# Optimization experiments

Measured on AMD Instinct MI355X. Metric: run time of the kernel, lower is better.

The kernel has to match this reference:

```python
import jax, jax.numpy as jnp
import numpy as np

DIM = 512
HEADS = 8
HEAD_DIM = DIM // HEADS
SR = 2
LN_EPS = 1e-3  # keras LayerNormalization default epsilon


def setup_inputs() -> dict:
    key = jax.random.key(0)
    ks = jax.random.split(key, 12)
    B, N = 4, 64 * 64
    s = lambda fan_in: 1.0 / np.sqrt(fan_in)
    return {
        "x": jax.random.normal(ks[0], (B, N, DIM), dtype=jnp.float32),
        "H": 64,
        "W": 64,
        "Wq": jax.random.normal(ks[1], (DIM, DIM), jnp.float32) * s(DIM),
        "bq": jnp.zeros((DIM,), jnp.float32),
        "Wkv": jax.random.normal(ks[2], (DIM, 2 * DIM), jnp.float32) * s(DIM),
        "bkv": jnp.zeros((2 * DIM,), jnp.float32),
        "Wp": jax.random.normal(ks[3], (DIM, DIM), jnp.float32) * s(DIM),
        "bp": jnp.zeros((DIM,), jnp.float32),
        "sr_kernel": jax.random.normal(ks[4], (SR, SR, DIM, DIM), jnp.float32) * s(SR * SR * DIM),
        "sr_bias": jnp.zeros((DIM,), jnp.float32),
        "gamma": jnp.ones((DIM,), jnp.float32),
        "beta": jnp.zeros((DIM,), jnp.float32),
    }


def _layer_norm(x, gamma, beta):
    mu = jnp.mean(x, axis=-1, keepdims=True)
    var = jnp.mean(jnp.square(x - mu), axis=-1, keepdims=True)
    return (x - mu) * jax.lax.rsqrt(var + LN_EPS) * gamma + beta


def reference(x, H, W, Wq, bq, Wkv, bkv, Wp, bp, sr_kernel, sr_bias, gamma, beta):
    B, N, C = x.shape
    scale = HEAD_DIM ** -0.5

    # q projection -> [B, heads, N, head_dim]
    q = (x @ Wq + bq).reshape(B, N, HEADS, HEAD_DIM).transpose(0, 2, 1, 3)

    # sequence reduction: strided conv (kernel=stride=SR, SAME padding) + LayerNorm
    x_ = x.reshape(B, H, W, C)
    x_ = jax.lax.conv_general_dilated(
        x_, sr_kernel, window_strides=(SR, SR), padding="SAME",
        dimension_numbers=("NHWC", "HWIO", "NHWC")) + sr_bias
    x_ = x_.reshape(B, -1, C)           # [B, N_kv, C]
    x_ = _layer_norm(x_, gamma, beta)

    # kv projection -> k, v: [B, heads, N_kv, head_dim]
    kv = (x_ @ Wkv + bkv).reshape(B, -1, 2, HEADS, HEAD_DIM).transpose(2, 0, 3, 1, 4)
    k, v = kv[0], kv[1]

    attn = jnp.einsum("bhnd,bhmd->bhnm", q, k) * scale
    attn = jax.nn.softmax(attn, axis=-1)
    out = jnp.einsum("bhnm,bhmd->bhnd", attn, v)  # [B, heads, N, head_dim]
    out = out.transpose(0, 2, 1, 3).reshape(B, N, C)
    return out @ Wp + bp
```

## Files before the change

### kernel.cpp

```cpp
#include <hip/hip_runtime.h>
#include <math.h>

#define BDIM   4
#define NTOK   4096
#define CDIM   512
#define NHEADS 8
#define HDIM   64
#define NKV    1024
#define HPIX   64
#define WPIX   64

typedef __attribute__((ext_vector_type(8)))  short    short8;
typedef __attribute__((ext_vector_type(4)))  float    floatx4;
typedef __attribute__((ext_vector_type(16))) float    floatx16;
typedef __attribute__((ext_vector_type(4)))  unsigned uintx4;
typedef unsigned short ushort_t;

static __device__ inline unsigned short f2bf(float f) {
  unsigned u = __float_as_uint(f);
  unsigned r = (u + 0x7fffu + ((u >> 16) & 1u)) >> 16;
  return (unsigned short)r;
}

static __device__ inline unsigned cvt_pk_bf16(float lo, float hi) {
  unsigned r;
  asm volatile("v_cvt_pk_bf16_f32 %0, %1, %2" : "=v"(r) : "v"(lo), "v"(hi));
  return r;
}

static __device__ inline void pl32_swap(unsigned& a, unsigned& b) {
  asm volatile("v_permlane32_swap_b32 %0, %1" : "+v"(a), "+v"(b));
}

static __device__ inline void gload16(const void* g, void* l) {
  __builtin_amdgcn_global_load_lds(
      (const __attribute__((address_space(1))) void*)g,
      (__attribute__((address_space(3))) void*)l, 16, 0, 0);
}

__global__ __launch_bounds__(256) void prep_kernel(
    const float* __restrict__ x, ushort_t* __restrict__ xb,
    const float* __restrict__ Wq, const float* __restrict__ Wkv,
    const float* __restrict__ Wp, const float* __restrict__ srk,
    ushort_t* __restrict__ Wqt, ushort_t* __restrict__ Wkvt,
    ushort_t* __restrict__ Wpt, ushort_t* __restrict__ srkt) {
  const int bid = blockIdx.x;
  if (bid < 4096) {
    const size_t i = ((size_t)bid * 256 + threadIdx.x) * 8;
    float4 f0 = *(const float4*)&x[i];
    float4 f1 = *(const float4*)&x[i + 4];
    short8 v;
    v[0] = (short)f2bf(f0.x); v[1] = (short)f2bf(f0.y);
    v[2] = (short)f2bf(f0.z); v[3] = (short)f2bf(f0.w);
    v[4] = (short)f2bf(f1.x); v[5] = (short)f2bf(f1.y);
    v[6] = (short)f2bf(f1.z); v[7] = (short)f2bf(f1.w);
    *(short8*)&xb[i] = v;
    return;
  }
  __shared__ float t[32][33];
  const int tb = bid - 4096;
  const float* in; ushort_t* outp; int C, tile;
  if (tb < 256)       { in = Wq;  outp = Wqt;  C = 512;  tile = tb; }
  else if (tb < 768)  { in = Wkv; outp = Wkvt; C = 1024; tile = tb - 256; }
  else if (tb < 1024) { in = Wp;  outp = Wpt;  C = 512;  tile = tb - 768; }
  else                { in = srk; outp = srkt; C = 512;  tile = tb - 1024; }
  const int R = (tb >= 1024) ? 2048 : 512;
  const int tcn = C >> 5;
  const int r0 = (tile / tcn) * 32, c0 = (tile % tcn) * 32;
  const int tr = threadIdx.x & 31, tc = threadIdx.x >> 5;
#pragma unroll
  for (int i = 0; i < 4; ++i)
    t[tc + 8 * i][tr] = in[(size_t)(r0 + tc + 8 * i) * C + c0 + tr];
  __syncthreads();
#pragma unroll
  for (int i = 0; i < 4; ++i)
    outp[(size_t)(c0 + tc + 8 * i) * R + r0 + tr] = f2bf(t[tr][tc + 8 * i]);
}

__global__ __launch_bounds__(256) void gemm_bf16(
    const ushort_t* __restrict__ A, const ushort_t* __restrict__ Bt,
    const float* __restrict__ bias, float* __restrict__ Cf,
    ushort_t* __restrict__ Cb, int M, int N, int K, float scale) {
  __shared__ char As[16384];
  __shared__ char Bs[16384];
  const int tid = threadIdx.x;
  const int w = tid >> 6, lane = tid & 63;
  const int g = lane >> 4, qr = lane & 15;
  const int wr = w >> 1, wc = w & 1;
  const int row0 = blockIdx.x * 128, col0 = blockIdx.y * 128;
  const int rl = w * 8 + (lane >> 3);
  const int sch = (lane & 7) ^ ((lane >> 3) & 7);

  floatx4 acc[4][4] = {};

  for (int k0 = 0; k0 < K; k0 += 64) {
    __syncthreads();
#pragma unroll
    for (int i = 0; i < 4; ++i) {
      const int r = rl + 32 * i;
      const unsigned lb = (unsigned)(w * 1024 + i * 4096);
      gload16(&A[(size_t)(row0 + r) * K + k0 + sch * 8], As + lb);
      gload16(&Bt[(size_t)(col0 + r) * K + k0 + sch * 8], Bs + lb);
    }
    __syncthreads();

#pragma unroll
    for (int kc = 0; kc < 2; ++kc) {
      short8 af[4], bfr[4];
#pragma unroll
      for (int mi = 0; mi < 4; ++mi) {
        const int r = wr * 64 + mi * 16 + qr;
        af[mi] = *(const short8*)(As +
            ((unsigned)(r * 128 + kc * 64 + g * 16) ^ (unsigned)((r & 7) << 4)));
      }
#pragma unroll
      for (int ni = 0; ni < 4; ++ni) {
        const int c = wc * 64 + ni * 16 + qr;
        bfr[ni] = *(const short8*)(Bs +
            ((unsigned)(c * 128 + kc * 64 + g * 16) ^ (unsigned)((c & 7) << 4)));
      }
#pragma unroll
      for (int mi = 0; mi < 4; ++mi)
#pragma unroll
        for (int ni = 0; ni < 4; ++ni)
          acc[mi][ni] = __builtin_amdgcn_mfma_f32_16x16x32_bf16(
              af[mi], bfr[ni], acc[mi][ni], 0, 0, 0);
    }
  }

#pragma unroll
  for (int mi = 0; mi < 4; ++mi) {
#pragma unroll
    for (int ni = 0; ni < 4; ++ni) {
      const int col = col0 + wc * 64 + ni * 16 + qr;
      const float bv = bias[col];
#pragma unroll
      for (int ri = 0; ri < 4; ++ri) {
        const int row = row0 + wr * 64 + mi * 16 + g * 4 + ri;
        const float v = (acc[mi][ni][ri] + bv) * scale;
        if (Cb) Cb[(size_t)row * N + col] = f2bf(v);
        else    Cf[(size_t)row * N + col] = v;
      }
    }
  }
}

__global__ __launch_bounds__(256) void qconv_gemm(
    const ushort_t* __restrict__ xb, const ushort_t* __restrict__ srkt,
    const float* __restrict__ srb, float* __restrict__ XR,
    const ushort_t* __restrict__ Wqt, const float* __restrict__ bq,
    ushort_t* __restrict__ Qb, float qscale) {
  __shared__ char As[16384];
  __shared__ char Bs[16384];
  const int tid = threadIdx.x;
  const int w = tid >> 6, lane = tid & 63;
  const int g = lane >> 4, qr = lane & 15;
  const int wr = w >> 1, wc = w & 1;
  const int rl = w * 8 + (lane >> 3);
  const int sch = (lane & 7) ^ ((lane >> 3) & 7);

  if (blockIdx.x < 256) {
    const int cb = blockIdx.x;
    const int row0 = (cb & 31) * 128, col0 = (cb >> 5) * 64;
    floatx4 acc[4][2] = {};

    for (int k0 = 0; k0 < 2048; k0 += 64) {
      __syncthreads();
      {
        const int di = k0 >> 10, dj = (k0 >> 9) & 1, cib = (k0 & 511) + sch * 8;
#pragma unroll
        for (int i = 0; i < 4; ++i) {
          const int r = rl + 32 * i;
          const int gr = row0 + r;
          const int bb = gr >> 10, p = gr & 1023;
          const int oi = p >> 5, oj = p & 31;
          const size_t off =
              ((size_t)((bb * HPIX + 2 * oi + di) * WPIX + 2 * oj + dj)) * CDIM + cib;
          gload16(&xb[off], As + (unsigned)(w * 1024 + i * 4096));
        }
#pragma unroll
        for (int i = 0; i < 2; ++i) {
          const int r = rl + 32 * i;
          gload16(&srkt[(size_t)(col0 + r) * 2048 + k0 + sch * 8],
                  Bs + (unsigned)(w * 1024 + i * 4096));
        }
      }
      __syncthreads();

#pragma unroll
      for (int kc = 0; kc < 2; ++kc) {
        short8 af[4], bfr[2];
#pragma unroll
        for (int mi = 0; mi < 4; ++mi) {
          const int r = wr * 64 + mi * 16 + qr;
          af[mi] = *(const short8*)(As +
              ((unsigned)(r * 128 + kc * 64 + g * 16) ^ (unsigned)((r & 7) << 4)));
        }
#pragma unroll
        for (int ni = 0; ni < 2; ++ni) {
          const int c = wc * 32 + ni * 16 + qr;
          bfr[ni] = *(const short8*)(Bs +
              ((unsigned)(c * 128 + kc * 64 + g * 16) ^ (unsigned)((c & 7) << 4)));
        }
#pragma unroll
        for (int mi = 0; mi < 4; ++mi)
#pragma unroll
          for (int ni = 0; ni < 2; ++ni)
            acc[mi][ni] = __builtin_amdgcn_mfma_f32_16x16x32_bf16(
                af[mi], bfr[ni], acc[mi][ni], 0, 0, 0);
      }
    }

#pragma unroll
    for (int mi = 0; mi < 4; ++mi) {
#pragma unroll
      for (int ni = 0; ni < 2; ++ni) {
        const int col = col0 + wc * 32 + ni * 16 + qr;
        const float bv = srb[col];
#pragma unroll
        for (int ri = 0; ri < 4; ++ri) {
          const int row = row0 + wr * 64 + mi * 16 + g * 4 + ri;
          XR[(size_t)row * 512 + col] = acc[mi][ni][ri] + bv;
        }
      }
    }
  } else {
    const int qb = blockIdx.x - 256;
    const int row0 = (qb & 127) * 128, col0 = (qb >> 7) * 128;
    floatx4 acc[4][4] = {};

    for (int k0 = 0; k0 < 512; k0 += 64) {
      __syncthreads();
#pragma unroll
      for (int i = 0; i < 4; ++i) {
        const int r = rl + 32 * i;
        const unsigned lb = (unsigned)(w * 1024 + i * 4096);
        gload16(&xb[(size_t)(row0 + r) * 512 + k0 + sch * 8], As + lb);
        gload16(&Wqt[(size_t)(col0 + r) * 512 + k0 + sch * 8], Bs + lb);
      }
      __syncthreads();

#pragma unroll
      for (int kc = 0; kc < 2; ++kc) {
        short8 af[4], bfr[4];
#pragma unroll
        for (int mi = 0; mi < 4; ++mi) {
          const int r = wr * 64 + mi * 16 + qr;
          af[mi] = *(const short8*)(As +
              ((unsigned)(r * 128 + kc * 64 + g * 16) ^ (unsigned)((r & 7) << 4)));
        }
#pragma unroll
        for (int ni = 0; ni < 4; ++ni) {
          const int c = wc * 64 + ni * 16 + qr;
          bfr[ni] = *(const short8*)(Bs +
              ((unsigned)(c * 128 + kc * 64 + g * 16) ^ (unsigned)((c & 7) << 4)));
        }
#pragma unroll
        for (int mi = 0; mi < 4; ++mi)
#pragma unroll
          for (int ni = 0; ni < 4; ++ni)
            acc[mi][ni] = __builtin_amdgcn_mfma_f32_16x16x32_bf16(
                af[mi], bfr[ni], acc[mi][ni], 0, 0, 0);
      }
    }

#pragma unroll
    for (int mi = 0; mi < 4; ++mi) {
#pragma unroll
      for (int ni = 0; ni < 4; ++ni) {
        const int col = col0 + wc * 64 + ni * 16 + qr;
        const float bv = bq[col];
#pragma unroll
        for (int ri = 0; ri < 4; ++ri) {
          const int row = row0 + wr * 64 + mi * 16 + g * 4 + ri;
          Qb[(size_t)row * 512 + col] = f2bf((acc[mi][ni][ri] + bv) * qscale);
        }
      }
    }
  }
}

__global__ __launch_bounds__(256) void gemm_kv(
    const ushort_t* __restrict__ A, const ushort_t* __restrict__ Bt,
    const float* __restrict__ bias, char* __restrict__ Kimg,
    char* __restrict__ Vimg) {
  __shared__ char As[16384];
  __shared__ char Bs[16384];
  const int tid = threadIdx.x;
  const int w = tid >> 6, lane = tid & 63;
  const int g = lane >> 4, qr = lane & 15;
  const int wr = w >> 1, wc = w & 1;
  const int row0 = blockIdx.x * 128, col0 = blockIdx.y * 128;
  const int rl = w * 8 + (lane >> 3);
  const int sch = (lane & 7) ^ ((lane >> 3) & 7);

  floatx4 acc[4][4] = {};

  for (int k0 = 0; k0 < 512; k0 += 64) {
    __syncthreads();
#pragma unroll
    for (int i = 0; i < 4; ++i) {
      const int r = rl + 32 * i;
      const unsigned lb = (unsigned)(w * 1024 + i * 4096);
      gload16(&A[(size_t)(row0 + r) * 512 + k0 + sch * 8], As + lb);
      gload16(&Bt[(size_t)(col0 + r) * 512 + k0 + sch * 8], Bs + lb);
    }
    __syncthreads();

#pragma unroll
    for (int kc = 0; kc < 2; ++kc) {
      short8 af[4], bfr[4];
#pragma unroll
      for (int mi = 0; mi < 4; ++mi) {
        const int r = wr * 64 + mi * 16 + qr;
        af[mi] = *(const short8*)(As +
            ((unsigned)(r * 128 + kc * 64 + g * 16) ^ (unsigned)((r & 7) << 4)));
      }
#pragma unroll
      for (int ni = 0; ni < 4; ++ni) {
        const int c = wc * 64 + ni * 16 + qr;
        bfr[ni] = *(const short8*)(Bs +
            ((unsigned)(c * 128 + kc * 64 + g * 16) ^ (unsigned)((c & 7) << 4)));
      }
#pragma unroll
      for (int mi = 0; mi < 4; ++mi)
#pragma unroll
        for (int ni = 0; ni < 4; ++ni)
          acc[mi][ni] = __builtin_amdgcn_mfma_f32_16x16x32_bf16(
              af[mi], bfr[ni], acc[mi][ni], 0, 0, 0);
    }
  }

#pragma unroll
  for (int mi = 0; mi < 4; ++mi) {
#pragma unroll
    for (int ni = 0; ni < 4; ++ni) {
      const int col = col0 + wc * 64 + ni * 16 + qr;
      const float bv = bias[col];
#pragma unroll
      for (int ri = 0; ri < 4; ++ri) {
        const int row = row0 + wr * 64 + mi * 16 + g * 4 + ri;
        const ushort_t v = f2bf(acc[mi][ni][ri] + bv);
        const int b = row >> 10, m = row & 1023;
        const int t = m >> 6, mr = m & 63;
        const int st = mr >> 5;
        if (col < 512) {
          const int h = col >> 6, d = col & 63;
          const int ql = mr & 31;
          const int ks = d >> 4, hi2 = (d >> 3) & 1, j = d & 7;
          char* img = Kimg + (((size_t)(b * NHEADS + h) * 16 + t) << 13);
          *(ushort_t*)(img + (unsigned)(((st * 4 + ks) << 10) +
                       ((hi2 << 5) + ql) * 16 + j * 2)) = v;
        } else {
          const int c = col - 512, h = c >> 6, d = c & 63;
          const int r5 = mr & 31;
          const int hf16 = r5 >> 4, rem = r5 & 15;
          const int hi2 = rem >> 3, cc = (rem >> 1) & 3, odd = rem & 1;
          const int db = d >> 5, ql = d & 31;
          char* img = Vimg + (((size_t)(b * NHEADS + h) * 16 + t) << 13);
          *(ushort_t*)(img + (unsigned)(((st * 4 + db * 2 + hf16) << 10) +
                       ((hi2 << 5) + ql) * 16 + cc * 4 + odd * 2)) = v;
        }
      }
    }
  }
}

__global__ __launch_bounds__(256) void ln_kernel(
    const float* __restrict__ in, ushort_t* __restrict__ out,
    const float* __restrict__ gamma, const float* __restrict__ beta) {
  const int row = blockIdx.x * 4 + (threadIdx.x >> 6);
  const int lane = threadIdx.x & 63;
  const float* p = in + (size_t)row * CDIM;
  float v[8];
  float s = 0.f;
#pragma unroll
  for (int j = 0; j < 8; ++j) { v[j] = p[lane + j * 64]; s += v[j]; }
#pragma unroll
  for (int o = 32; o > 0; o >>= 1) s += __shfl_xor(s, o);
  const float mu = s * (1.0f / 512.0f);
  float vs = 0.f;
#pragma unroll
  for (int j = 0; j < 8; ++j) { const float d = v[j] - mu; vs += d * d; }
#pragma unroll
  for (int o = 32; o > 0; o >>= 1) vs += __shfl_xor(vs, o);
  const float rstd = rsqrtf(vs * (1.0f / 512.0f) + 1e-3f);
  ushort_t* q = out + (size_t)row * CDIM;
#pragma unroll
  for (int j = 0; j < 8; ++j) {
    const int c = lane + j * 64;
    q[c] = f2bf((v[j] - mu) * rstd * gamma[c] + beta[c]);
  }
}

__global__ __launch_bounds__(256) void attn_kernel(
    const ushort_t* __restrict__ Q, const char* __restrict__ Kimg,
    const char* __restrict__ Vimg, ushort_t* __restrict__ AO) {
  __shared__ char Ks[16384];
  __shared__ char Vt[16384];

  const int b = blockIdx.z, h = blockIdx.y;
  const int q0 = blockIdx.x * 128;
  const int tid = threadIdx.x;
  const int w = tid >> 6, lane = tid & 63;
  const int ql = lane & 31;
  const int hi = lane >> 5;
  const unsigned lbyte = (unsigned)(lane * 16);

  short8 qf[4];
  {
    const ushort_t* qp = &Q[((size_t)(b * NTOK + q0 + 32 * w + ql)) * CDIM + h * HDIM];
#pragma unroll
    for (int ks = 0; ks < 4; ++ks)
      qf[ks] = *(const short8*)&qp[ks * 16 + hi * 8];
  }

  short8 ones;
#pragma unroll
  for (int i = 0; i < 8; ++i) ones[i] = (short)0x3F80;

  const char* kbase = Kimg + (((size_t)(b * NHEADS + h)) << 17);
  const char* vbase = Vimg + (((size_t)(b * NHEADS + h)) << 17);

  floatx16 Oacc[2] = {};
  floatx16 Lacc = {};

  for (int t2 = 0; t2 < NKV / 128; ++t2) {
    __syncthreads();
    {
      const char* kg = kbase + ((size_t)t2 << 14) + w * 4096 + lane * 16;
      const char* vg = vbase + ((size_t)t2 << 14) + w * 4096 + lane * 16;
      char* kd = Ks + w * 4096;
      char* vd = Vt + w * 4096;
#pragma unroll
      for (int i = 0; i < 4; ++i) {
        gload16(kg + i * 1024, kd + i * 1024);
        gload16(vg + i * 1024, vd + i * 1024);
      }
    }
    __syncthreads();

#pragma unroll
    for (int sub = 0; sub < 2; ++sub) {
      const char* ksb = Ks + sub * 8192 + lbyte;
      const char* vtb = Vt + sub * 8192 + lbyte;

      floatx16 sacc[2];
      __builtin_amdgcn_s_setprio(1);
#pragma unroll
      for (int st = 0; st < 2; ++st) {
        floatx16 s_ = {};
#pragma unroll
        for (int ks = 0; ks < 4; ++ks) {
          short8 kf = *(const short8*)(ksb + ((st * 4 + ks) << 10));
          s_ = __builtin_amdgcn_mfma_f32_32x32x16_bf16(kf, qf[ks], s_, 0, 0, 0);
        }
        sacc[st] = s_;
      }
      __builtin_amdgcn_s_setprio(0);

#pragma unroll
      for (int st = 0; st < 2; ++st) {
        unsigned W[8];
#pragma unroll
        for (int i = 0; i < 8; ++i) {
          const float pa = __builtin_amdgcn_exp2f(sacc[st][2 * i]);
          const float pb = __builtin_amdgcn_exp2f(sacc[st][2 * i + 1]);
          W[i] = cvt_pk_bf16(pa, pb);
        }
        pl32_swap(W[0], W[2]); pl32_swap(W[1], W[3]);
        pl32_swap(W[4], W[6]); pl32_swap(W[5], W[7]);
        uintx4 u0 = {W[0], W[1], W[2], W[3]};
        uintx4 u1 = {W[4], W[5], W[6], W[7]};
        const short8 pa0 = __builtin_bit_cast(short8, u0);
        const short8 pa1 = __builtin_bit_cast(short8, u1);
        __builtin_amdgcn_s_setprio(1);
#pragma unroll
        for (int db = 0; db < 2; ++db) {
          short8 v0 = *(const short8*)(vtb + ((st * 4 + db * 2) << 10));
          short8 v1 = *(const short8*)(vtb + ((st * 4 + db * 2 + 1) << 10));
          Oacc[db] = __builtin_amdgcn_mfma_f32_32x32x16_bf16(pa0, v0, Oacc[db], 0, 0, 0);
          Oacc[db] = __builtin_amdgcn_mfma_f32_32x32x16_bf16(pa1, v1, Oacc[db], 0, 0, 0);
        }
        Lacc = __builtin_amdgcn_mfma_f32_32x32x16_bf16(pa0, ones, Lacc, 0, 0, 0);
        Lacc = __builtin_amdgcn_mfma_f32_32x32x16_bf16(pa1, ones, Lacc, 0, 0, 0);
        __builtin_amdgcn_s_setprio(0);
      }
    }
  }

#pragma unroll
  for (int r = 0; r < 16; ++r) {
    const int qrow = (r & 3) + 8 * (r >> 2) + 4 * hi;
    const float iv = 1.0f / Lacc[r];
    const size_t rowoff =
        ((size_t)(b * NTOK + q0 + 32 * w + qrow)) * CDIM + h * HDIM;
    AO[rowoff + ql]      = f2bf(Oacc[0][r] * iv);
    AO[rowoff + 32 + ql] = f2bf(Oacc[1][r] * iv);
  }
}

extern "C" void kernel_launch(void* const* d_in, const int* in_sizes, int n_in,
                              void* d_out, int out_size, void* d_ws, size_t ws_size,
                              hipStream_t stream) {
  const float* x     = (const float*)d_in[0];
  const float* Wq    = (const float*)d_in[3];
  const float* bq    = (const float*)d_in[4];
  const float* Wkv   = (const float*)d_in[5];
  const float* bkv   = (const float*)d_in[6];
  const float* Wp    = (const float*)d_in[7];
  const float* bp    = (const float*)d_in[8];
  const float* srk   = (const float*)d_in[9];
  const float* srb   = (const float*)d_in[10];
  const float* gamma = (const float*)d_in[11];
  const float* beta  = (const float*)d_in[12];
  float* out = (float*)d_out;

  ushort_t* xb   = (ushort_t*)d_ws;
  ushort_t* Qb   = xb + (size_t)16384 * 512;
  ushort_t* AOb  = Qb + (size_t)16384 * 512;
  float*    XR   = (float*)(AOb + (size_t)16384 * 512);
  ushort_t* XL   = (ushort_t*)(XR + (size_t)4096 * 512);
  char*     Kimg = (char*)(XL + (size_t)4096 * 512);
  char*     Vimg = Kimg + (size_t)4 * 8 * 16 * 8192;
  ushort_t* Wqt  = (ushort_t*)(Vimg + (size_t)4 * 8 * 16 * 8192);
  ushort_t* Wkvt = Wqt + (size_t)512 * 512;
  ushort_t* Wpt  = Wkvt + (size_t)1024 * 512;
  ushort_t* srkt = Wpt + (size_t)512 * 512;

  prep_kernel<<<4096 + 2048, 256, 0, stream>>>(
      x, xb, Wq, Wkv, Wp, srk, Wqt, Wkvt, Wpt, srkt);

  qconv_gemm<<<768, 256, 0, stream>>>(
      xb, srkt, srb, XR, Wqt, bq, Qb, 0.125f * 1.44269504f);
  ln_kernel<<<4096 / 4, 256, 0, stream>>>(XR, XL, gamma, beta);
  gemm_kv<<<dim3(4096 / 128, 1024 / 128), 256, 0, stream>>>(
      XL, Wkvt, bkv, Kimg, Vimg);
  attn_kernel<<<dim3(NTOK / 128, NHEADS, BDIM), 256, 0, stream>>>(Qb, Kimg, Vimg, AOb);
  gemm_bf16<<<dim3(16384 / 128, 512 / 128), 256, 0, stream>>>(
      AOb, Wpt, bp, out, nullptr, 16384, 512, 512, 1.0f);
}
```

Before: 126.6 us.

## Process 64 query rows per wave in attention to reuse K/V tiles

```diff
diff --git a/kernel.cpp b/kernel.cpp
--- a/kernel.cpp
+++ b/kernel.cpp
@@ -400,19 +400,21 @@
   __shared__ char Vt[16384];
 
   const int b = blockIdx.z, h = blockIdx.y;
-  const int q0 = blockIdx.x * 128;
+  const int q0 = blockIdx.x * 256;
   const int tid = threadIdx.x;
   const int w = tid >> 6, lane = tid & 63;
   const int ql = lane & 31;
   const int hi = lane >> 5;
   const unsigned lbyte = (unsigned)(lane * 16);
 
-  short8 qf[4];
-  {
-    const ushort_t* qp = &Q[((size_t)(b * NTOK + q0 + 32 * w + ql)) * CDIM + h * HDIM];
+  short8 qf[2][4];
+#pragma unroll
+  for (int half = 0; half < 2; ++half) {
+    const ushort_t* qp =
+        &Q[((size_t)(b * NTOK + q0 + 64 * w + 32 * half + ql)) * CDIM + h * HDIM];
 #pragma unroll
     for (int ks = 0; ks < 4; ++ks)
-      qf[ks] = *(const short8*)&qp[ks * 16 + hi * 8];
+      qf[half][ks] = *(const short8*)&qp[ks * 16 + hi * 8];
   }
 
   short8 ones;
@@ -422,8 +424,8 @@
   const char* kbase = Kimg + (((size_t)(b * NHEADS + h)) << 17);
   const char* vbase = Vimg + (((size_t)(b * NHEADS + h)) << 17);
 
-  floatx16 Oacc[2] = {};
-  floatx16 Lacc = {};
+  floatx16 Oacc[2][2] = {};
+  floatx16 Lacc[2] = {};
 
   for (int t2 = 0; t2 < NKV / 128; ++t2) {
     __syncthreads();
@@ -445,58 +447,73 @@
       const char* ksb = Ks + sub * 8192 + lbyte;
       const char* vtb = Vt + sub * 8192 + lbyte;
 
-      floatx16 sacc[2];
-      __builtin_amdgcn_s_setprio(1);
 #pragma unroll
       for (int st = 0; st < 2; ++st) {
-        floatx16 s_ = {};
+        floatx16 s0 = {}, s1 = {};
+        __builtin_amdgcn_s_setprio(1);
 #pragma unroll
         for (int ks = 0; ks < 4; ++ks) {
           short8 kf = *(const short8*)(ksb + ((st * 4 + ks) << 10));
-          s_ = __builtin_amdgcn_mfma_f32_32x32x16_bf16(kf, qf[ks], s_, 0, 0, 0);
-        }
-        sacc[st] = s_;
-      }
-      __builtin_amdgcn_s_setprio(0);
-
-#pragma unroll
-      for (int st = 0; st < 2; ++st) {
-        unsigned W[8];
-#pragma unroll
-        for (int i = 0; i < 8; ++i) {
-          const float pa = __builtin_amdgcn_exp2f(sacc[st][2 * i]);
-          const float pb = __builtin_amdgcn_exp2f(sacc[st][2 * i + 1]);
-          W[i] = cvt_pk_bf16(pa, pb);
-        }
-        pl32_swap(W[0], W[2]); pl32_swap(W[1], W[3]);
-        pl32_swap(W[4], W[6]); pl32_swap(W[5], W[7]);
-        uintx4 u0 = {W[0], W[1], W[2], W[3]};
-        uintx4 u1 = {W[4], W[5], W[6], W[7]};
-        const short8 pa0 = __builtin_bit_cast(short8, u0);
-        const short8 pa1 = __builtin_bit_cast(short8, u1);
+          s0 = __builtin_amdgcn_mfma_f32_32x32x16_bf16(kf, qf[0][ks], s0, 0, 0, 0);
+          s1 = __builtin_amdgcn_mfma_f32_32x32x16_bf16(kf, qf[1][ks], s1, 0, 0, 0);
+        }
+        __builtin_amdgcn_s_setprio(0);
+
+        short8 pa0[2], pa1[2];
+#pragma unroll
+        for (int half = 0; half < 2; ++half) {
+          const floatx16 sv = half ? s1 : s0;
+          unsigned W[8];
+#pragma unroll
+          for (int i = 0; i < 8; ++i) {
+            const float pa = __builtin_amdgcn_exp2f(sv[2 * i]);
+            const float pb = __builtin_amdgcn_exp2f(sv[2 * i + 1]);
+            W[i] = cvt_pk_bf16(pa, pb);
+          }
+          pl32_swap(W[0], W[2]); pl32_swap(W[1], W[3]);
+          pl32_swap(W[4], W[6]); pl32_swap(W[5], W[7]);
+          uintx4 u0 = {W[0], W[1], W[2], W[3]};
+          uintx4 u1 = {W[4], W[5], W[6], W[7]};
+          pa0[half] = __builtin_bit_cast(short8, u0);
+          pa1[half] = __builtin_bit_cast(short8, u1);
+        }
+
         __builtin_amdgcn_s_setprio(1);
 #pragma unroll
         for (int db = 0; db < 2; ++db) {
           short8 v0 = *(const short8*)(vtb + ((st * 4 + db * 2) << 10));
           short8 v1 = *(const short8*)(vtb + ((st * 4 + db * 2 + 1) << 10));
-          Oacc[db] = __builtin_amdgcn_mfma_f32_32x32x16_bf16(pa0, v0, Oacc[db], 0, 0, 0);
-          Oacc[db] = __builtin_amdgcn_mfma_f32_32x32x16_bf16(pa1, v1, Oacc[db], 0, 0, 0);
-        }
-        Lacc = __builtin_amdgcn_mfma_f32_32x32x16_bf16(pa0, ones, Lacc, 0, 0, 0);
-        Lacc = __builtin_amdgcn_mfma_f32_32x32x16_bf16(pa1, ones, Lacc, 0, 0, 0);
+#pragma unroll
+          for (int half = 0; half < 2; ++half) {
+            Oacc[half][db] = __builtin_amdgcn_mfma_f32_32x32x16_bf16(
+                pa0[half], v0, Oacc[half][db], 0, 0, 0);
+            Oacc[half][db] = __builtin_amdgcn_mfma_f32_32x32x16_bf16(
+                pa1[half], v1, Oacc[half][db], 0, 0, 0);
+          }
+        }
+#pragma unroll
+        for (int half = 0; half < 2; ++half) {
+          Lacc[half] = __builtin_amdgcn_mfma_f32_32x32x16_bf16(
+              pa0[half], ones, Lacc[half], 0, 0, 0);
+          Lacc[half] = __builtin_amdgcn_mfma_f32_32x32x16_bf16(
+              pa1[half], ones, Lacc[half], 0, 0, 0);
+        }
         __builtin_amdgcn_s_setprio(0);
       }
     }
   }
 
 #pragma unroll
-  for (int r = 0; r < 16; ++r) {
-    const int qrow = (r & 3) + 8 * (r >> 2) + 4 * hi;
-    const float iv = 1.0f / Lacc[r];
-    const size_t rowoff =
-        ((size_t)(b * NTOK + q0 + 32 * w + qrow)) * CDIM + h * HDIM;
-    AO[rowoff + ql]      = f2bf(Oacc[0][r] * iv);
-    AO[rowoff + 32 + ql] = f2bf(Oacc[1][r] * iv);
+  for (int half = 0; half < 2; ++half) {
+#pragma unroll
+    for (int r = 0; r < 16; ++r) {
+      const int qrow = (r & 3) + 8 * (r >> 2) + 4 * hi;
+      const float iv = 1.0f / Lacc[half][r];
+      const size_t rowoff =
+          ((size_t)(b * NTOK + q0 + 64 * w + 32 * half + qrow)) * CDIM + h * HDIM;
+      AO[rowoff + ql]      = f2bf(Oacc[half][0][r] * iv);
+      AO[rowoff + 32 + ql] = f2bf(Oacc[half][1][r] * iv);
+    }
   }
 }
 
@@ -536,7 +553,7 @@
   ln_kernel<<<4096 / 4, 256, 0, stream>>>(XR, XL, gamma, beta);
   gemm_kv<<<dim3(4096 / 128, 1024 / 128), 256, 0, stream>>>(
       XL, Wkvt, bkv, Kimg, Vimg);
-  attn_kernel<<<dim3(NTOK / 128, NHEADS, BDIM), 256, 0, stream>>>(Qb, Kimg, Vimg, AOb);
+  attn_kernel<<<dim3(NTOK / 256, NHEADS, BDIM), 256, 0, stream>>>(Qb, Kimg, Vimg, AOb);
   gemm_bf16<<<dim3(16384 / 128, 512 / 128), 256, 0, stream>>>(
       AOb, Wpt, bp, out, nullptr, 16384, 512, 512, 1.0f);
 }
```

Result: slower. 136.5 us (+7.8%).
